# Kernel tuning notes

Measured on AMD Instinct MI355X. Metric: run time of the kernel, lower is better.

## Reference

```python
import jax, jax.numpy as jnp
import numpy as np
import math

MODEL_DIM = 2048
NUM_Q_HEADS = 32
NUM_KV_HEADS = 8
HEAD_DIM = 64
ROPE_BASE = 10000.0
RMS_EPS = 1e-6


def setup_inputs() -> dict:
    key = jax.random.key(0)
    k1, k2, k3 = jax.random.split(key, 3)
    B, S = 2, 2048
    std = MODEL_DIM ** -0.5
    qkv_out = (NUM_Q_HEADS + 2 * NUM_KV_HEADS) * HEAD_DIM  # 3072
    return {
        "x": jax.random.normal(k1, (B, S, MODEL_DIM), dtype=jnp.float32),
        "w_qkv": jax.random.normal(k2, (qkv_out, MODEL_DIM), dtype=jnp.float32) * std,
        "w_out": jax.random.normal(k3, (MODEL_DIM, NUM_Q_HEADS * HEAD_DIM), dtype=jnp.float32) * std,
        "q_gamma": jnp.ones((HEAD_DIM,), dtype=jnp.float32),
        "k_gamma": jnp.ones((HEAD_DIM,), dtype=jnp.float32),
    }


def _rms_norm(x, gamma):
    # weight * sqrt(d) * F.normalize(x, dim=-1, eps): x / max(||x||_2, eps)
    norm = jnp.sqrt(jnp.sum(x * x, axis=-1, keepdims=True))
    scale = HEAD_DIM ** 0.5
    return (gamma * scale) * x / jnp.maximum(norm, RMS_EPS)


def _rope(x):
    # x: [B, H, S, hd]; rotate-half style RoPE, offset=0
    S = x.shape[2]
    half = HEAD_DIM // 2
    pos = jnp.arange(S, dtype=x.dtype)
    freqs = jnp.exp(-jnp.arange(half, dtype=x.dtype) * (math.log(ROPE_BASE) / half))
    theta = pos[:, None] * freqs[None, :]  # [S, half]
    sin, cos = jnp.sin(theta), jnp.cos(theta)
    x1, x2 = x[..., :half], x[..., half:]
    return jnp.concatenate([x1 * cos - x2 * sin, x1 * sin + x2 * cos], axis=-1)


def reference(x, w_qkv, w_out, q_gamma, k_gamma):
    B, S, D = x.shape
    groups = NUM_Q_HEADS // NUM_KV_HEADS
    qkv = jnp.einsum("bsd,ed->bse", x, w_qkv)  # [B,S,3072]
    qkv = qkv.reshape(B, S, NUM_Q_HEADS + 2 * NUM_KV_HEADS, HEAD_DIM).transpose(0, 2, 1, 3)
    q = qkv[:, :NUM_Q_HEADS]                                 # [B,Hq,S,hd]
    k = qkv[:, NUM_Q_HEADS:NUM_Q_HEADS + NUM_KV_HEADS]       # [B,Hk,S,hd]
    v = qkv[:, NUM_Q_HEADS + NUM_KV_HEADS:]                  # [B,Hk,S,hd]
    q = _rope(_rms_norm(q, q_gamma))
    k = _rope(_rms_norm(k, k_gamma))
    # GQA: repeat_interleave over head dim
    k = jnp.repeat(k, groups, axis=1)  # [B,Hq,S,hd]
    v = jnp.repeat(v, groups, axis=1)
    scale = 1.0 / (HEAD_DIM ** 0.5)
    scores = jnp.einsum("bhqd,bhkd->bhqk", q, k) * scale
    causal = jnp.tril(jnp.ones((S, S), dtype=bool))
    scores = jnp.where(causal, scores, jnp.finfo(scores.dtype).min)
    attn = jax.nn.softmax(scores, axis=-1)
    out = jnp.einsum("bhqk,bhkd->bhqd", attn, v)             # [B,Hq,S,hd]
    out = out.transpose(0, 2, 1, 3).reshape(B, S, NUM_Q_HEADS * HEAD_DIM)
    return jnp.einsum("bse,de->bsd", out, w_out)
```

## Files before the change

### kernel.cpp

```cpp
#include <hip/hip_runtime.h>
#include <hip/hip_bf16.h>
#include <stdint.h>

#define S_LEN  2048
#define BATCH  2
#define DMODEL 2048
#define EQKV   3072
#define HQ     32
#define HKV    8
#define HD     64
#define MROWS  (BATCH * S_LEN)

typedef unsigned short u16;
typedef __attribute__((ext_vector_type(8))) short bf16x8;
typedef __attribute__((ext_vector_type(4))) short bf16x4;
typedef __attribute__((ext_vector_type(4))) float f32x4;

__device__ __forceinline__ u16 f2bf(float f) {
  uint32_t x = __builtin_bit_cast(uint32_t, f);
  uint32_t r = x + 0x7fffu + ((x >> 16) & 1u);
  return (u16)(r >> 16);
}
__device__ __forceinline__ short f2bf_s(float f) {
  return __builtin_bit_cast(short, __float2bfloat16(f));
}
__device__ __forceinline__ float b2f(u16 u) {
  uint32_t x = ((uint32_t)u) << 16;
  return __builtin_bit_cast(float, x);
}
__device__ __forceinline__ float bflo(uint32_t u) {
  uint32_t x = u << 16; return __builtin_bit_cast(float, x);
}
__device__ __forceinline__ float bfhi(uint32_t u) {
  uint32_t x = u & 0xffff0000u; return __builtin_bit_cast(float, x);
}
__device__ __forceinline__ float fexp2(float x) {
#if __has_builtin(__builtin_amdgcn_exp2f)
  return __builtin_amdgcn_exp2f(x);
#else
  return exp2f(x);
#endif
}

__device__ __forceinline__ void gld16(const void* g, void* l) {
  __builtin_amdgcn_global_load_lds(
      (const __attribute__((address_space(1))) void*)g,
      (__attribute__((address_space(3))) void*)l, 16, 0, 0);
}

#define N8_X  ((size_t)MROWS * DMODEL / 8)
#define N8_WQ ((size_t)EQKV * DMODEL / 8)
#define N8_WO ((size_t)DMODEL * DMODEL / 8)
__global__ void cast3(const float* __restrict__ xa, const float* __restrict__ xb,
                      const float* __restrict__ xc,
                      u16* __restrict__ oa, u16* __restrict__ ob, u16* __restrict__ oc) {
  const int ntot = (int)(N8_X + N8_WQ + N8_WO);
  int stride = gridDim.x * blockDim.x;
  for (int i = blockIdx.x * blockDim.x + threadIdx.x; i < ntot; i += stride) {
    const float* in;
    u16* out;
    int j = i;
    if (j < (int)N8_X)                { in = xa; out = oa; }
    else if (j < (int)(N8_X + N8_WQ)) { in = xb; out = ob; j -= (int)N8_X; }
    else                              { in = xc; out = oc; j -= (int)(N8_X + N8_WQ); }
    const float4* p = (const float4*)(in + (size_t)j * 8);
    float4 a = p[0], b = p[1];
    uint32_t u0 = (uint32_t)f2bf(a.x) | ((uint32_t)f2bf(a.y) << 16);
    uint32_t u1 = (uint32_t)f2bf(a.z) | ((uint32_t)f2bf(a.w) << 16);
    uint32_t u2 = (uint32_t)f2bf(b.x) | ((uint32_t)f2bf(b.y) << 16);
    uint32_t u3 = (uint32_t)f2bf(b.z) | ((uint32_t)f2bf(b.w) << 16);
    *(uint4*)(out + (size_t)j * 8) = make_uint4(u0, u1, u2, u3);
  }
}

template<int OUT_BF16>
__global__ __launch_bounds__(512) void gemm_bt(const u16* __restrict__ A,
                                               const u16* __restrict__ Bm,
                                               void* __restrict__ Cv,
                                               int M, int N, int K, int nbx) {
  __shared__ u16 lA[128 * 64];
  __shared__ u16 lB[128 * 64];
  const int tid  = threadIdx.x;
  const int wave = tid >> 6;
  const int lane = tid & 63;

  const int nwg = gridDim.x;
  const int wg  = blockIdx.x;
  const int swz = (wg & 7) * (nwg >> 3) + (wg >> 3);
  const int brow = (swz % nbx) * 128;
  const int bcol = (swz / nbx) * 128;

  const int wr = (wave >> 2) * 64;
  const int wc = (wave & 3) * 32;
  const int fr = lane & 15;
  const int fq = lane >> 4;

  const int srow8 = lane >> 3;
  const int scol  = ((lane & 7) ^ srow8) * 8;

  f32x4 acc[4][2];
#pragma unroll
  for (int i = 0; i < 4; ++i)
#pragma unroll
    for (int j = 0; j < 2; ++j) acc[i][j] = (f32x4){0.f, 0.f, 0.f, 0.f};

  for (int k0 = 0; k0 < K; k0 += 64) {
    __syncthreads();
#pragma unroll
    for (int j = 0; j < 2; ++j) {
      int c = wave * 2 + j;
      int r = c * 8 + srow8;
      gld16(A  + (size_t)(brow + r) * K + k0 + scol, (char*)lA + c * 1024);
      gld16(Bm + (size_t)(bcol + r) * K + k0 + scol, (char*)lB + c * 1024);
    }
    __syncthreads();

    bf16x8 af[2][4], bfr[2][2];
#pragma unroll
    for (int kc = 0; kc < 2; ++kc) {
#pragma unroll
      for (int i = 0; i < 4; ++i) {
        int row = wr + i * 16 + fr;
        af[kc][i] = *(const bf16x8*)&lA[row * 64 + (((kc * 4 + fq) ^ (row & 7)) << 3)];
      }
#pragma unroll
      for (int j = 0; j < 2; ++j) {
        int row = wc + j * 16 + fr;
        bfr[kc][j] = *(const bf16x8*)&lB[row * 64 + (((kc * 4 + fq) ^ (row & 7)) << 3)];
      }
    }
#pragma unroll
    for (int kc = 0; kc < 2; ++kc)
#pragma unroll
      for (int i = 0; i < 4; ++i)
#pragma unroll
        for (int j = 0; j < 2; ++j)
          acc[i][j] = __builtin_amdgcn_mfma_f32_16x16x32_bf16(af[kc][i], bfr[kc][j], acc[i][j], 0, 0, 0);
  }

#pragma unroll
  for (int i = 0; i < 4; ++i)
#pragma unroll
    for (int j = 0; j < 2; ++j)
#pragma unroll
      for (int v = 0; v < 4; ++v) {
        int row = brow + wr + i * 16 + fq * 4 + v;
        int col = bcol + wc + j * 16 + fr;
        float val = acc[i][j][v];
        if (OUT_BF16) ((u16*)Cv)[(size_t)row * N + col] = f2bf(val);
        else          ((float*)Cv)[(size_t)row * N + col] = val;
      }
}

__global__ __launch_bounds__(256) void rmsrope(const u16* __restrict__ qkv,
                                               u16* __restrict__ Qb,
                                               u16* __restrict__ Kb,
                                               const float* __restrict__ qg,
                                               const float* __restrict__ kg) {
  int wid  = blockIdx.x * 4 + (threadIdx.x >> 6);
  int lane = threadIdx.x & 63;
  int head = wid % 40;
  int bs   = wid / 40;
  int s    = bs & (S_LEN - 1);
  int b    = bs >> 11;

  float v = b2f(qkv[(size_t)bs * EQKV + head * HD + lane]);
  float ss = v * v;
#pragma unroll
  for (int msk = 32; msk >= 1; msk >>= 1) ss += __shfl_xor(ss, msk);
  float norm = sqrtf(ss);
  float g = (head < 32) ? qg[lane] : kg[lane];
  float xv = v * (8.0f * g / fmaxf(norm, 1e-6f));
  float prt = __shfl_xor(xv, 32);
  int i = lane & 31;
  float freq  = expf(-(float)i * 0.28782313662425572f);
  float theta = (float)s * freq;
  float sn = sinf(theta), cs = cosf(theta);
  float res = (lane < 32) ? (xv * cs - prt * sn) : (prt * sn + xv * cs);
  u16 r = f2bf(res);
  if (head < 32) Qb[(((size_t)(b * HQ  + head     )) * S_LEN + s) * HD + lane] = r;
  else           Kb[(((size_t)(b * HKV + head - 32)) * S_LEN + s) * HD + lane] = r;
}

__global__ __launch_bounds__(256) void vtrans(const u16* __restrict__ qkv,
                                              u16* __restrict__ VTb) {
  __shared__ u16 T[64][68];
  const int bid   = blockIdx.x;
  const int stile = bid & 31;
  const int plane = bid >> 5;
  const int b = plane >> 3, kh = plane & 7;
  const int s0 = stile * 64;
  const int t = threadIdx.x;
  const int r = t >> 2, u0 = t & 3;

  const u16* src = qkv + ((size_t)(b * S_LEN + s0 + r)) * EQKV + (HQ + HKV + kh) * HD;
  *(uint4*)&T[r][u0 * 8]      = *(const uint4*)(src + u0 * 8);
  *(uint4*)&T[r][u0 * 8 + 32] = *(const uint4*)(src + u0 * 8 + 32);
  __syncthreads();

  const int d = t >> 2;
  u16* dst = VTb + ((size_t)plane * HD + d) * S_LEN + s0;
#pragma unroll
  for (int half = 0; half < 2; ++half) {
    int ub = u0 + half * 4;
    u16 tmp[8];
#pragma unroll
    for (int j = 0; j < 8; ++j) tmp[j] = T[ub * 8 + j][d];
    *(uint4*)(dst + ub * 8) = *(const uint4*)tmp;
  }
}

__global__ __launch_bounds__(128) void attn_mfma(const u16* __restrict__ Qb,
                                                 const u16* __restrict__ Kb,
                                                 const u16* __restrict__ VTb,
                                                 u16* __restrict__ Ob) {
  __shared__ u16 Ks[64 * 64];
  __shared__ u16 Vt[64 * 64];
  const int tid  = threadIdx.x;
  const int wv   = tid >> 6;
  const int lane = tid & 63;
  const int fr   = lane & 15;
  const int fq   = lane >> 4;
  const int bh   = blockIdx.x;
  const int b    = bh >> 5, h = bh & 31, kh = h >> 2;
  const size_t kvbase = ((size_t)(b * HKV + kh)) * S_LEN * HD;

  const int tile   = 31 - (int)blockIdx.y;
  const int wqmin  = tile * 64 + wv * 32;
  const int kv_end = tile * 64 + 64;

  const int srow  = lane >> 3;
  const int sunit = (lane & 7) ^ srow;
  const u16* kp0 = Kb  + kvbase + (size_t)(wv * 32 + srow) * HD    + sunit * 8;
  const u16* vp0 = VTb + kvbase + (size_t)(wv * 32 + srow) * S_LEN + sunit * 8;

  const float QSCALE = 0.18033688011112042f;
  bf16x8 aq[2][2];
#pragma unroll
  for (int qf = 0; qf < 2; ++qf)
#pragma unroll
    for (int kc = 0; kc < 2; ++kc) {
      const u16* qp = Qb + ((size_t)bh * S_LEN + (wqmin + qf * 16 + fr)) * HD + kc * 32 + fq * 8;
      uint4 u = *(const uint4*)qp;
      uint32_t w[4] = {u.x, u.y, u.z, u.w};
      bf16x8 r;
#pragma unroll
      for (int i = 0; i < 4; ++i) {
        r[2 * i]     = f2bf_s(bflo(w[i]) * QSCALE);
        r[2 * i + 1] = f2bf_s(bfhi(w[i]) * QSCALE);
      }
      aq[qf][kc] = r;
    }

  const f32x4 Z4 = (f32x4){0.f, 0.f, 0.f, 0.f};
  bf16x4 ones;
#pragma unroll
  for (int v = 0; v < 4; ++v) ones[v] = (short)0x3F80;

  f32x4 o[2][4];
#pragma unroll
  for (int qf = 0; qf < 2; ++qf)
#pragma unroll
    for (int df = 0; df < 4; ++df) o[qf][df] = Z4;
  f32x4 lacc[2] = {Z4, Z4};

  for (int k0 = 0; k0 < kv_end; k0 += 64) {
    __syncthreads();
#pragma unroll
    for (int i = 0; i < 4; ++i)
      gld16(kp0 + (size_t)(k0 + i * 8) * HD, (char*)Ks + (wv * 4 + i) * 1024);
#pragma unroll
    for (int i = 0; i < 4; ++i)
      gld16(vp0 + k0 + (size_t)(i * 8) * S_LEN, (char*)Vt + (wv * 4 + i) * 1024);
    __syncthreads();

    f32x4 st[2][4];
    __builtin_amdgcn_s_setprio(1);
#pragma unroll
    for (int kf = 0; kf < 4; ++kf) {
      int row = kf * 16 + fr;
      bf16x8 ak0 = *(const bf16x8*)((char*)Ks + row * 128 +
                                    ((fq * 16) ^ ((row & 7) << 4)));
      bf16x8 ak1 = *(const bf16x8*)((char*)Ks + row * 128 +
                                    ((64 + fq * 16) ^ ((row & 7) << 4)));
#pragma unroll
      for (int qf = 0; qf < 2; ++qf) {
        f32x4 t = __builtin_amdgcn_mfma_f32_16x16x32_bf16(ak0, aq[qf][0], Z4, 0, 0, 0);
        st[qf][kf] = __builtin_amdgcn_mfma_f32_16x16x32_bf16(ak1, aq[qf][1], t, 0, 0, 0);
      }
    }
    __builtin_amdgcn_s_setprio(0);

    const bool need_mask = (k0 + 63 > wqmin);
    bf16x4 pb[2][4];
#pragma unroll
    for (int qf = 0; qf < 2; ++qf) {
      const int qrow = wqmin + qf * 16 + fr;
      if (need_mask) {
#pragma unroll
        for (int kf = 0; kf < 4; ++kf)
#pragma unroll
          for (int v = 0; v < 4; ++v) {
            int kvg = k0 + kf * 16 + fq * 4 + v;
            st[qf][kf][v] = (kvg > qrow) ? -1e30f : st[qf][kf][v];
          }
      }
#pragma unroll
      for (int kf = 0; kf < 4; ++kf) {
        bf16x4 pp;
#pragma unroll
        for (int v = 0; v < 4; ++v) pp[v] = f2bf_s(fexp2(st[qf][kf][v]));
        pb[qf][kf] = pp;
      }
    }

    __builtin_amdgcn_s_setprio(1);
#pragma unroll
    for (int df = 0; df < 4; ++df) {
      int row = df * 16 + fr;
#pragma unroll
      for (int kf = 0; kf < 4; ++kf) {
        bf16x4 av = *(const bf16x4*)((char*)Vt + row * 128 +
                                     ((kf * 32 + fq * 8) ^ ((row & 7) << 4)));
#pragma unroll
        for (int qf = 0; qf < 2; ++qf)
          o[qf][df] = __builtin_amdgcn_mfma_f32_16x16x16bf16_1k(av, pb[qf][kf], o[qf][df], 0, 0, 0);
      }
    }
#pragma unroll
    for (int kf = 0; kf < 4; ++kf)
#pragma unroll
      for (int qf = 0; qf < 2; ++qf)
        lacc[qf] = __builtin_amdgcn_mfma_f32_16x16x16bf16_1k(ones, pb[qf][kf], lacc[qf], 0, 0, 0);
    __builtin_amdgcn_s_setprio(0);
  }

#pragma unroll
  for (int qf = 0; qf < 2; ++qf) {
    float inv = 1.0f / lacc[qf][0];
    int grow = b * S_LEN + wqmin + qf * 16 + fr;
#pragma unroll
    for (int df = 0; df < 4; ++df) {
      u16* op = Ob + (size_t)grow * DMODEL + h * HD + df * 16 + fq * 4;
      uint32_t w0 = (uint32_t)f2bf(o[qf][df][0] * inv) | ((uint32_t)f2bf(o[qf][df][1] * inv) << 16);
      uint32_t w1 = (uint32_t)f2bf(o[qf][df][2] * inv) | ((uint32_t)f2bf(o[qf][df][3] * inv) << 16);
      *(uint2*)op = make_uint2(w0, w1);
    }
  }
}

extern "C" void kernel_launch(void* const* d_in, const int* in_sizes, int n_in,
                              void* d_out, int out_size, void* d_ws, size_t ws_size,
                              hipStream_t stream) {
  const float* x    = (const float*)d_in[0];
  const float* wqkv = (const float*)d_in[1];
  const float* wout = (const float*)d_in[2];
  const float* qg   = (const float*)d_in[3];
  const float* kg   = (const float*)d_in[4];
  float* out = (float*)d_out;
  char* ws = (char*)d_ws;

  const size_t MB = 1024 * 1024;
  u16* xb    = (u16*)(ws + 0 * MB);
  u16* wqkvb = (u16*)(ws + 16 * MB);
  u16* qkvb  = (u16*)(ws + 28 * MB);
  u16* Qb    = (u16*)(ws + 52 * MB);
  u16* Kb    = (u16*)(ws + 68 * MB);
  u16* VTb   = (u16*)(ws + 72 * MB);
  u16* Ob    = xb;
  u16* woutb = (u16*)(ws + 76 * MB);

  cast3<<<2048, 256, 0, stream>>>(x, wqkv, wout, xb, wqkvb, woutb);
  gemm_bt<1><<<(MROWS / 128) * (EQKV / 128), 512, 0, stream>>>(xb, wqkvb, qkvb, MROWS, EQKV, DMODEL, MROWS / 128);
  rmsrope<<<(MROWS * 40) / 4, 256, 0, stream>>>(qkvb, Qb, Kb, qg, kg);
  vtrans<<<BATCH * HKV * 32, 256, 0, stream>>>(qkvb, VTb);
  attn_mfma<<<dim3(BATCH * HQ, 32), 128, 0, stream>>>(Qb, Kb, VTb, Ob);
  gemm_bt<0><<<(MROWS / 128) * (DMODEL / 128), 512, 0, stream>>>(Ob, woutb, out, MROWS, DMODEL, DMODEL, MROWS / 128);
}
```

Baseline: 211.0 us.

## Double-buffer K/V tiles in LDS to prefetch the next tile during compute

The attention kernel now keeps two LDS buffers each for K and V. It issues the async global-to-LDS loads for the next KV tile before computing the current one, and uses one barrier per iteration instead of two. The goal is to hide global load latency behind the QK and PV MFMA work. The cost is double the LDS per block, which can lower the number of resident blocks per CU.

```diff
diff --git a/kernel.cpp b/kernel.cpp
--- a/kernel.cpp
+++ b/kernel.cpp
@@ -214,8 +214,8 @@
                                                  const u16* __restrict__ Kb,
                                                  const u16* __restrict__ VTb,
                                                  u16* __restrict__ Ob) {
-  __shared__ u16 Ks[64 * 64];
-  __shared__ u16 Vt[64 * 64];
+  __shared__ u16 Ks[2][64 * 64];
+  __shared__ u16 Vt[2][64 * 64];
   const int tid  = threadIdx.x;
   const int wv   = tid >> 6;
   const int lane = tid & 63;
@@ -227,7 +227,7 @@
 
   const int tile   = 31 - (int)blockIdx.y;
   const int wqmin  = tile * 64 + wv * 32;
-  const int kv_end = tile * 64 + 64;
+  const int nt     = tile + 1;
 
   const int srow  = lane >> 3;
   const int sunit = (lane & 7) ^ srow;
@@ -264,29 +264,39 @@
     for (int df = 0; df < 4; ++df) o[qf][df] = Z4;
   f32x4 lacc[2] = {Z4, Z4};
 
-  for (int k0 = 0; k0 < kv_end; k0 += 64) {
+#pragma unroll
+  for (int i = 0; i < 4; ++i) {
+    gld16(kp0 + (size_t)(i * 8) * HD,    (char*)Ks[0] + (wv * 4 + i) * 1024);
+    gld16(vp0 + (size_t)(i * 8) * S_LEN, (char*)Vt[0] + (wv * 4 + i) * 1024);
+  }
+
+  for (int t = 0; t < nt; ++t) {
+    const int cur = t & 1;
+    const int k0  = t * 64;
     __syncthreads();
-#pragma unroll
-    for (int i = 0; i < 4; ++i)
-      gld16(kp0 + (size_t)(k0 + i * 8) * HD, (char*)Ks + (wv * 4 + i) * 1024);
-#pragma unroll
-    for (int i = 0; i < 4; ++i)
-      gld16(vp0 + k0 + (size_t)(i * 8) * S_LEN, (char*)Vt + (wv * 4 + i) * 1024);
-    __syncthreads();
+
+    if (t + 1 < nt) {
+      const int nk0 = k0 + 64;
+#pragma unroll
+      for (int i = 0; i < 4; ++i) {
+        gld16(kp0 + (size_t)(nk0 + i * 8) * HD,    (char*)Ks[cur ^ 1] + (wv * 4 + i) * 1024);
+        gld16(vp0 + nk0 + (size_t)(i * 8) * S_LEN, (char*)Vt[cur ^ 1] + (wv * 4 + i) * 1024);
+      }
+    }
 
     f32x4 st[2][4];
     __builtin_amdgcn_s_setprio(1);
 #pragma unroll
     for (int kf = 0; kf < 4; ++kf) {
       int row = kf * 16 + fr;
-      bf16x8 ak0 = *(const bf16x8*)((char*)Ks + row * 128 +
+      bf16x8 ak0 = *(const bf16x8*)((char*)Ks[cur] + row * 128 +
                                     ((fq * 16) ^ ((row & 7) << 4)));
-      bf16x8 ak1 = *(const bf16x8*)((char*)Ks + row * 128 +
+      bf16x8 ak1 = *(const bf16x8*)((char*)Ks[cur] + row * 128 +
                                     ((64 + fq * 16) ^ ((row & 7) << 4)));
 #pragma unroll
       for (int qf = 0; qf < 2; ++qf) {
-        f32x4 t = __builtin_amdgcn_mfma_f32_16x16x32_bf16(ak0, aq[qf][0], Z4, 0, 0, 0);
-        st[qf][kf] = __builtin_amdgcn_mfma_f32_16x16x32_bf16(ak1, aq[qf][1], t, 0, 0, 0);
+        f32x4 tt = __builtin_amdgcn_mfma_f32_16x16x32_bf16(ak0, aq[qf][0], Z4, 0, 0, 0);
+        st[qf][kf] = __builtin_amdgcn_mfma_f32_16x16x32_bf16(ak1, aq[qf][1], tt, 0, 0, 0);
       }
     }
     __builtin_amdgcn_s_setprio(0);
@@ -320,7 +330,7 @@
       int row = df * 16 + fr;
 #pragma unroll
       for (int kf = 0; kf < 4; ++kf) {
-        bf16x4 av = *(const bf16x4*)((char*)Vt + row * 128 +
+        bf16x4 av = *(const bf16x4*)((char*)Vt[cur] + row * 128 +
                                      ((kf * 32 + fq * 8) ^ ((row & 7) << 4)));
 #pragma unroll
         for (int qf = 0; qf < 2; ++qf)
```

Result: slower. 221.7 us (+5.1%).
